# Kernel tuning notes

Hardware: AMD Instinct MI355X
Metric: run time of the kernel (lower is better)

Reference implementation:

```python
import jax, jax.numpy as jnp
import numpy as np

N_NODES = 100000


def _deg_isqrt(idx, n):
    # clamped-to-1 degree, then ^-0.5 (DGL GraphConv norm='both')
    deg = jax.ops.segment_sum(jnp.ones(idx.shape, jnp.float32), idx, num_segments=n)
    return jnp.power(jnp.maximum(deg, 1.0), -0.5)


def _graph_conv(feat, W, b, src, dst, out_isqrt, in_isqrt, n):
    # norm='both': scale by src out-degree^-1/2, mult-first (in>out), spmm, scale by dst in-degree^-1/2
    h = (feat * out_isqrt[:, None]) @ W                      # [N, out]
    h = jax.ops.segment_sum(h[src], dst, num_segments=n)     # gather/scatter over edges
    return h * in_isqrt[:, None] + b


def setup_inputs() -> dict:
    key = jax.random.key(0)
    ks = jax.random.split(key, 10)
    in_dim, h1, h2 = 512, 64, 32
    n, e = N_NODES, 800000
    features = jax.random.normal(ks[0], (n, in_dim), jnp.float32)
    src = jax.random.randint(ks[1], (e,), 0, n)
    dst = jax.random.randint(ks[2], (e,), 0, n)
    noise = jax.random.normal(ks[3], (n, h2), jnp.float32)
    s1 = 1.0 / np.sqrt(in_dim)
    s2 = 1.0 / np.sqrt(h1)
    W1 = jax.random.uniform(ks[4], (in_dim, h1), jnp.float32, -s1, s1)
    b1 = jnp.zeros((h1,), jnp.float32)
    W2 = jax.random.uniform(ks[5], (h1, h2), jnp.float32, -s2, s2)
    b2 = jnp.zeros((h2,), jnp.float32)
    W3 = jax.random.uniform(ks[6], (h1, h2), jnp.float32, -s2, s2)
    b3 = jnp.zeros((h2,), jnp.float32)
    return {"features": features, "src": src, "dst": dst, "noise": noise,
            "W1": W1, "b1": b1, "W2": W2, "b2": b2, "W3": W3, "b3": b3}


def reference(features, src, dst, noise, W1, b1, W2, b2, W3, b3):
    n = features.shape[0]
    out_isqrt = _deg_isqrt(src, n)
    in_isqrt = _deg_isqrt(dst, n)
    h = jax.nn.relu(_graph_conv(features, W1, b1, src, dst, out_isqrt, in_isqrt, n))
    mean = _graph_conv(h, W2, b2, src, dst, out_isqrt, in_isqrt, n)
    log_std = _graph_conv(h, W3, b3, src, dst, out_isqrt, in_isqrt, n)
    z = mean + noise * jnp.exp(log_std)
    return z, mean, log_std
```

## Files before the change

kernel.cpp:

```cpp
#include <hip/hip_runtime.h>
#include <hip/hip_bf16.h>


typedef __attribute__((ext_vector_type(8))) short short8;
typedef __attribute__((ext_vector_type(4))) float f32x4;
typedef unsigned short ushort_t;

static __device__ inline short f2bf(float f)
{
    union { __hip_bfloat16 h; short s; } u;
    u.h = __float2bfloat16(f);
    return u.s;
}

static __device__ inline float bf2f(ushort_t u)
{
    union { float f; unsigned v; } w;
    w.v = ((unsigned)u) << 16;
    return w.f;
}

static __device__ inline short8 cvt8(float4 lo, float4 hi)
{
    short8 r;
    r[0] = f2bf(lo.x); r[1] = f2bf(lo.y); r[2] = f2bf(lo.z); r[3] = f2bf(lo.w);
    r[4] = f2bf(hi.x); r[5] = f2bf(hi.y); r[6] = f2bf(hi.z); r[7] = f2bf(hi.w);
    return r;
}

__global__ __launch_bounds__(256) void k_setup(
    const float* __restrict__ W1, const float* __restrict__ W2,
    const float* __restrict__ W3, short* __restrict__ w1f,
    float* __restrict__ wc, int4* __restrict__ zp, int z4)
{
    int gid = blockIdx.x * 256 + threadIdx.x;
    if (gid < z4) zp[gid] = make_int4(0, 0, 0, 0);
    if (gid < 64 * 64) {
        int k = gid >> 6, c = gid & 63;
        wc[gid] = (c < 32) ? W2[k * 32 + c] : W3[k * 32 + (c - 32)];
    }
    if (gid < 512 * 64) {
        int k = gid >> 6, c = gid & 63;
        int kt = k >> 5, kk = k & 31, nt = c >> 4, lr = c & 15;
        int kg = kk >> 3, j = kk & 7;
        int l = kg * 16 + lr;
        w1f[(kt * 4 + nt) * 512 + l * 8 + j] = f2bf(W1[gid]);
    }
}

__global__ __launch_bounds__(256) void k_deg_int(
    const int* __restrict__ src, const int* __restrict__ dst,
    int* __restrict__ degS, int* __restrict__ degD, int e)
{
    int gid = blockIdx.x * 256 + threadIdx.x;
    if (gid >= e) return;
    atomicAdd(&degS[src[gid]], 1);
    atomicAdd(&degD[dst[gid]], 1);
}

__global__ __launch_bounds__(256) void k_scan_block_sums(
    const int* __restrict__ deg, int* __restrict__ partials, int n)
{
    __shared__ int red[256];
    int gid = blockIdx.x * 256 + threadIdx.x;
    red[threadIdx.x] = (gid < n) ? deg[gid] : 0;
    __syncthreads();
    for (int s = 128; s > 0; s >>= 1) {
        if (threadIdx.x < s) red[threadIdx.x] += red[threadIdx.x + s];
        __syncthreads();
    }
    if (threadIdx.x == 0) partials[blockIdx.x] = red[0];
}

__global__ __launch_bounds__(512) void k_scan_partials(
    int* __restrict__ partials, int nb)
{
    __shared__ int s[512];
    int t = threadIdx.x;
    s[t] = (t < nb) ? partials[t] : 0;
    __syncthreads();
    for (int d = 1; d < 512; d <<= 1) {
        int v = (t >= d) ? s[t - d] : 0;
        __syncthreads();
        s[t] += v;
        __syncthreads();
    }
    if (t < nb) partials[t] = (t == 0) ? 0 : s[t - 1];
}

__global__ __launch_bounds__(256) void k_scan_final(
    const int* __restrict__ degD, const int* __restrict__ degS,
    const int* __restrict__ partials,
    int* __restrict__ row_ptr, int* __restrict__ cursor,
    float* __restrict__ isq_out, float* __restrict__ isq_in, int n)
{
    __shared__ int s[256];
    int t = threadIdx.x;
    int gid = blockIdx.x * 256 + t;
    int v = (gid < n) ? degD[gid] : 0;
    s[t] = v;
    __syncthreads();
    for (int d = 1; d < 256; d <<= 1) {
        int u = (t >= d) ? s[t - d] : 0;
        __syncthreads();
        s[t] += u;
        __syncthreads();
    }
    int start = partials[blockIdx.x] + s[t] - v;
    if (gid < n) {
        row_ptr[gid] = start;
        cursor[gid]  = start;
        isq_in[gid]  = 1.0f / sqrtf((float)max(v, 1));
        isq_out[gid] = 1.0f / sqrtf((float)max(degS[gid], 1));
    }
    if (gid == n - 1) row_ptr[n] = start + v;
}

__global__ __launch_bounds__(256) void k_scatter(
    const int* __restrict__ src, const int* __restrict__ dst,
    int* __restrict__ cursor, int* __restrict__ edge_src, int e)
{
    int gid = blockIdx.x * 256 + threadIdx.x;
    if (gid >= e) return;
    int pos = atomicAdd(&cursor[dst[gid]], 1);
    edge_src[pos] = src[gid];
}

__global__ __launch_bounds__(256) void k_gemm1_mfma(
    const float* __restrict__ X, const short* __restrict__ w1f,
    const float* __restrict__ scale, ushort_t* __restrict__ Y, int n)
{
    const int tid  = threadIdx.x;
    const int l    = tid & 63;
    const int wv   = tid >> 6;
    const int row0 = blockIdx.x * 128 + wv * 32;
    const int lr   = l & 15;
    const int kg   = l >> 4;

    int ra0 = row0 + lr;       if (ra0 >= n) ra0 = n - 1;
    int ra1 = row0 + 16 + lr;  if (ra1 >= n) ra1 = n - 1;
    const float* pa0 = X + (size_t)ra0 * 512 + kg * 8;
    const float* pa1 = X + (size_t)ra1 * 512 + kg * 8;
    const short* pb  = w1f + l * 8;

    f32x4 acc[2][4];
#pragma unroll
    for (int i = 0; i < 2; ++i)
#pragma unroll
        for (int j = 0; j < 4; ++j) acc[i][j] = (f32x4){0.f, 0.f, 0.f, 0.f};

    float4 a0lo = *(const float4*)(pa0);
    float4 a0hi = *(const float4*)(pa0 + 4);
    float4 a1lo = *(const float4*)(pa1);
    float4 a1hi = *(const float4*)(pa1 + 4);
    short8 b0 = *(const short8*)(pb);
    short8 b1 = *(const short8*)(pb + 512);
    short8 b2 = *(const short8*)(pb + 1024);
    short8 b3 = *(const short8*)(pb + 1536);

    for (int kt = 0; kt < 16; ++kt) {
        short8 ca0 = cvt8(a0lo, a0hi);
        short8 ca1 = cvt8(a1lo, a1hi);
        short8 cb0 = b0, cb1 = b1, cb2 = b2, cb3 = b3;

        if (kt < 15) {
            const float* q0 = pa0 + (kt + 1) * 32;
            const float* q1 = pa1 + (kt + 1) * 32;
            a0lo = *(const float4*)(q0);
            a0hi = *(const float4*)(q0 + 4);
            a1lo = *(const float4*)(q1);
            a1hi = *(const float4*)(q1 + 4);
            const short* q = pb + (size_t)(kt + 1) * 2048;
            b0 = *(const short8*)(q);
            b1 = *(const short8*)(q + 512);
            b2 = *(const short8*)(q + 1024);
            b3 = *(const short8*)(q + 1536);
        }

        acc[0][0] = __builtin_amdgcn_mfma_f32_16x16x32_bf16(ca0, cb0, acc[0][0], 0, 0, 0);
        acc[0][1] = __builtin_amdgcn_mfma_f32_16x16x32_bf16(ca0, cb1, acc[0][1], 0, 0, 0);
        acc[0][2] = __builtin_amdgcn_mfma_f32_16x16x32_bf16(ca0, cb2, acc[0][2], 0, 0, 0);
        acc[0][3] = __builtin_amdgcn_mfma_f32_16x16x32_bf16(ca0, cb3, acc[0][3], 0, 0, 0);
        acc[1][0] = __builtin_amdgcn_mfma_f32_16x16x32_bf16(ca1, cb0, acc[1][0], 0, 0, 0);
        acc[1][1] = __builtin_amdgcn_mfma_f32_16x16x32_bf16(ca1, cb1, acc[1][1], 0, 0, 0);
        acc[1][2] = __builtin_amdgcn_mfma_f32_16x16x32_bf16(ca1, cb2, acc[1][2], 0, 0, 0);
        acc[1][3] = __builtin_amdgcn_mfma_f32_16x16x32_bf16(ca1, cb3, acc[1][3], 0, 0, 0);
    }

#pragma unroll
    for (int mr = 0; mr < 2; ++mr) {
#pragma unroll
        for (int m = 0; m < 4; ++m) {
            int row = row0 + mr * 16 + kg * 4 + m;
            if (row < n) {
                float s = scale[row];
#pragma unroll
                for (int nt = 0; nt < 4; ++nt)
                    Y[(size_t)row * 64 + nt * 16 + lr] =
                        (ushort_t)f2bf(acc[mr][nt][m] * s);
            }
        }
    }
}

__global__ __launch_bounds__(256) void k_gather_h(
    const int* __restrict__ row_ptr, const int* __restrict__ edge_src,
    const ushort_t* __restrict__ x, const float* __restrict__ isq_in,
    const float* __restrict__ isq_out, const float* __restrict__ b1,
    float* __restrict__ h, int n)
{
    int col  = threadIdx.x & 63;
    int node = __builtin_amdgcn_readfirstlane(blockIdx.x * 4 + (threadIdx.x >> 6));
    if (node >= n) return;
    int j = row_ptr[node], jend = row_ptr[node + 1];
    float a0 = 0.f, a1 = 0.f, a2 = 0.f, a3 = 0.f;
    float a4 = 0.f, a5 = 0.f, a6 = 0.f, a7 = 0.f;
    for (; j + 7 < jend; j += 8) {
        int e0 = edge_src[j],     e1 = edge_src[j + 1];
        int e2 = edge_src[j + 2], e3 = edge_src[j + 3];
        int e4 = edge_src[j + 4], e5 = edge_src[j + 5];
        int e6 = edge_src[j + 6], e7 = edge_src[j + 7];
        a0 += bf2f(x[(size_t)e0 * 64 + col]);
        a1 += bf2f(x[(size_t)e1 * 64 + col]);
        a2 += bf2f(x[(size_t)e2 * 64 + col]);
        a3 += bf2f(x[(size_t)e3 * 64 + col]);
        a4 += bf2f(x[(size_t)e4 * 64 + col]);
        a5 += bf2f(x[(size_t)e5 * 64 + col]);
        a6 += bf2f(x[(size_t)e6 * 64 + col]);
        a7 += bf2f(x[(size_t)e7 * 64 + col]);
    }
    for (; j + 1 < jend; j += 2) {
        int e0 = edge_src[j], e1 = edge_src[j + 1];
        a0 += bf2f(x[(size_t)e0 * 64 + col]);
        a1 += bf2f(x[(size_t)e1 * 64 + col]);
    }
    if (j < jend) a2 += bf2f(x[(size_t)edge_src[j] * 64 + col]);
    float acc = ((a0 + a1) + (a2 + a3)) + ((a4 + a5) + (a6 + a7));
    h[(size_t)node * 64 + col] =
        fmaxf(acc * isq_in[node] + b1[col], 0.f) * isq_out[node];
}

__global__ __launch_bounds__(256) void k_gemm2(
    const float* __restrict__ X, const float* __restrict__ W,
    ushort_t* __restrict__ Y, int n)
{
    __shared__ float sx[64][68];
    __shared__ float sw[64][64];
    const int tid  = threadIdx.x;
    const int colp = tid & 31;
    const int rg   = tid >> 5;
    const int row0 = blockIdx.x * 64;

    float2 acc[8];
#pragma unroll
    for (int i = 0; i < 8; ++i) acc[i] = make_float2(0.f, 0.f);

#pragma unroll
    for (int p = 0; p < 4; ++p) {
        int u = p * 256 + tid;
        int r = u >> 4, c4 = (u & 15) * 4;
        int row = row0 + r;
        float4 v = make_float4(0.f, 0.f, 0.f, 0.f);
        if (row < n) v = *(const float4*)&X[(size_t)row * 64 + c4];
        *(float4*)&sx[r][c4] = v;
        *(float4*)&sw[r][c4] = *(const float4*)&W[u * 4];
    }
    __syncthreads();

#pragma unroll 4
    for (int k4 = 0; k4 < 64; k4 += 4) {
        float2 w0 = *(const float2*)&sw[k4 + 0][colp * 2];
        float2 w1 = *(const float2*)&sw[k4 + 1][colp * 2];
        float2 w2 = *(const float2*)&sw[k4 + 2][colp * 2];
        float2 w3 = *(const float2*)&sw[k4 + 3][colp * 2];
#pragma unroll
        for (int i = 0; i < 8; ++i) {
            float4 f = *(const float4*)&sx[rg * 8 + i][k4];
            acc[i].x += f.x * w0.x + f.y * w1.x + f.z * w2.x + f.w * w3.x;
            acc[i].y += f.x * w0.y + f.y * w1.y + f.z * w2.y + f.w * w3.y;
        }
    }

#pragma unroll
    for (int i = 0; i < 8; ++i) {
        int row = row0 + rg * 8 + i;
        if (row < n) {
            unsigned lo = (unsigned)(unsigned short)f2bf(acc[i].x);
            unsigned hi = (unsigned)(unsigned short)f2bf(acc[i].y);
            ((unsigned*)Y)[(size_t)row * 32 + colp] = (hi << 16) | lo;
        }
    }
}

__global__ __launch_bounds__(256) void k_gather_final(
    const int* __restrict__ row_ptr, const int* __restrict__ edge_src,
    const ushort_t* __restrict__ t23, const float* __restrict__ isq_in,
    const float* __restrict__ b2, const float* __restrict__ b3,
    const float* __restrict__ noise, float* __restrict__ out, int n)
{
    int lane = threadIdx.x & 63;
    int node = __builtin_amdgcn_readfirstlane(blockIdx.x * 4 + (threadIdx.x >> 6));
    if (node >= n) return;
    int j = row_ptr[node], jend = row_ptr[node + 1];
    float a0 = 0.f, a1 = 0.f, a2 = 0.f, a3 = 0.f;
    float a4 = 0.f, a5 = 0.f, a6 = 0.f, a7 = 0.f;
    for (; j + 7 < jend; j += 8) {
        int e0 = edge_src[j],     e1 = edge_src[j + 1];
        int e2 = edge_src[j + 2], e3 = edge_src[j + 3];
        int e4 = edge_src[j + 4], e5 = edge_src[j + 5];
        int e6 = edge_src[j + 6], e7 = edge_src[j + 7];
        a0 += bf2f(t23[(size_t)e0 * 64 + lane]);
        a1 += bf2f(t23[(size_t)e1 * 64 + lane]);
        a2 += bf2f(t23[(size_t)e2 * 64 + lane]);
        a3 += bf2f(t23[(size_t)e3 * 64 + lane]);
        a4 += bf2f(t23[(size_t)e4 * 64 + lane]);
        a5 += bf2f(t23[(size_t)e5 * 64 + lane]);
        a6 += bf2f(t23[(size_t)e6 * 64 + lane]);
        a7 += bf2f(t23[(size_t)e7 * 64 + lane]);
    }
    for (; j + 1 < jend; j += 2) {
        int e0 = edge_src[j], e1 = edge_src[j + 1];
        a0 += bf2f(t23[(size_t)e0 * 64 + lane]);
        a1 += bf2f(t23[(size_t)e1 * 64 + lane]);
    }
    if (j < jend) a2 += bf2f(t23[(size_t)edge_src[j] * 64 + lane]);
    float acc = ((a0 + a1) + (a2 + a3)) + ((a4 + a5) + (a6 + a7));
    float si = isq_in[node];
    float v  = acc * si + (lane < 32 ? b2[lane] : b3[lane - 32]);
    float lv = __shfl(v, lane | 32, 64);
    int total = n * 32;
    int base  = node * 32 + (lane & 31);
    if (lane < 32) {
        float z = v + noise[base] * expf(lv);
        out[base]         = z;
        out[total + base] = v;
    } else {
        out[2 * total + base] = v;
    }
}

extern "C" void kernel_launch(void* const* d_in, const int* in_sizes, int n_in,
                              void* d_out, int out_size, void* d_ws, size_t ws_size,
                              hipStream_t stream)
{
    const float* feat  = (const float*)d_in[0];
    const int*   src   = (const int*)d_in[1];
    const int*   dst   = (const int*)d_in[2];
    const float* noise = (const float*)d_in[3];
    const float* W1    = (const float*)d_in[4];
    const float* b1    = (const float*)d_in[5];
    const float* W2    = (const float*)d_in[6];
    const float* b2    = (const float*)d_in[7];
    const float* W3    = (const float*)d_in[8];
    const float* b3    = (const float*)d_in[9];

    const int n = in_sizes[0] / 512;
    const int e = in_sizes[1];

    float* ws      = (float*)d_ws;
    float* isq_out = ws;
    float* isq_in  = ws + n;
    float* bufA    = ws + 2 * (size_t)n;
    float* bufB    = bufA + 64 * (size_t)n;
    float* wc      = bufB + 64 * (size_t)n;
    short* w1f     = (short*)(wc + 64 * 64);
    int*   ip      = (int*)(w1f + 512 * 64);
    int* row_ptr   = ip;
    int* cursor    = ip + (n + 1);
    int* partials  = cursor + n;
    int* edge_src  = partials + 512;
    int* degS = (int*)bufA;
    int* degD = degS + n;
    float* out = (float*)d_out;

    const int nb = (n + 255) / 256;
    const int z4 = (2 * n) / 4;

    k_setup<<<(z4 + 255) / 256, 256, 0, stream>>>(
        W1, W2, W3, w1f, wc, (int4*)degS, z4);

    k_deg_int<<<(e + 255) / 256, 256, 0, stream>>>(src, dst, degS, degD, e);

    k_scan_block_sums<<<nb, 256, 0, stream>>>(degD, partials, n);
    k_scan_partials<<<1, 512, 0, stream>>>(partials, nb);
    k_scan_final<<<nb, 256, 0, stream>>>(
        degD, degS, partials, row_ptr, cursor, isq_out, isq_in, n);
    k_scatter<<<(e + 255) / 256, 256, 0, stream>>>(src, dst, cursor, edge_src, e);

    k_gemm1_mfma<<<(n + 127) / 128, 256, 0, stream>>>(
        feat, w1f, isq_out, (ushort_t*)bufA, n);

    k_gather_h<<<(n + 3) / 4, 256, 0, stream>>>(
        row_ptr, edge_src, (const ushort_t*)bufA, isq_in, isq_out, b1, bufB, n);

    k_gemm2<<<(n + 63) / 64, 256, 0, stream>>>(bufB, wc, (ushort_t*)bufA, n);

    k_gather_final<<<(n + 3) / 4, 256, 0, stream>>>(
        row_ptr, edge_src, (const ushort_t*)bufA, isq_in, b2, b3, noise, out, n);
}
```

Baseline: 282.0 us.

## Halve rows per wave in gemm1, double-buffer A loads, hoist gather scalar loads

The first MFMA GEMM now gives each wave 16 rows instead of 32 and launches twice as many blocks. It also prefetches A two K-steps ahead using alternating register buffers and fully unrolls the K loop. The aim is more waves and deeper load pipelining for the bandwidth-bound 512-wide feature read. In the gather kernels, per-node scale, bias and noise loads move ahead of the edge loop so their latency overlaps the gathers. The trade-off is that each B-operand (W1) load is now reused over half as many rows, which raises weight traffic per output row.

```diff
diff --git a/kernel.cpp b/kernel.cpp
--- a/kernel.cpp
+++ b/kernel.cpp
@@ -133,72 +133,58 @@
     const int tid  = threadIdx.x;
     const int l    = tid & 63;
     const int wv   = tid >> 6;
-    const int row0 = blockIdx.x * 128 + wv * 32;
+    const int row0 = (blockIdx.x * 4 + wv) * 16;
     const int lr   = l & 15;
     const int kg   = l >> 4;
 
-    int ra0 = row0 + lr;       if (ra0 >= n) ra0 = n - 1;
-    int ra1 = row0 + 16 + lr;  if (ra1 >= n) ra1 = n - 1;
-    const float* pa0 = X + (size_t)ra0 * 512 + kg * 8;
-    const float* pa1 = X + (size_t)ra1 * 512 + kg * 8;
-    const short* pb  = w1f + l * 8;
-
-    f32x4 acc[2][4];
-#pragma unroll
-    for (int i = 0; i < 2; ++i)
-#pragma unroll
-        for (int j = 0; j < 4; ++j) acc[i][j] = (f32x4){0.f, 0.f, 0.f, 0.f};
-
-    float4 a0lo = *(const float4*)(pa0);
-    float4 a0hi = *(const float4*)(pa0 + 4);
-    float4 a1lo = *(const float4*)(pa1);
-    float4 a1hi = *(const float4*)(pa1 + 4);
+    int ra = row0 + lr;  if (ra >= n) ra = n - 1;
+    const float* pa = X + (size_t)ra * 512 + kg * 8;
+    const short* pb = w1f + l * 8;
+
+    f32x4 acc[4];
+#pragma unroll
+    for (int j = 0; j < 4; ++j) acc[j] = (f32x4){0.f, 0.f, 0.f, 0.f};
+
+    float4 alo0 = *(const float4*)(pa);
+    float4 ahi0 = *(const float4*)(pa + 4);
+    float4 alo1 = *(const float4*)(pa + 32);
+    float4 ahi1 = *(const float4*)(pa + 36);
     short8 b0 = *(const short8*)(pb);
     short8 b1 = *(const short8*)(pb + 512);
     short8 b2 = *(const short8*)(pb + 1024);
     short8 b3 = *(const short8*)(pb + 1536);
 
+#pragma unroll
     for (int kt = 0; kt < 16; ++kt) {
-        short8 ca0 = cvt8(a0lo, a0hi);
-        short8 ca1 = cvt8(a1lo, a1hi);
+        short8 ca = (kt & 1) ? cvt8(alo1, ahi1) : cvt8(alo0, ahi0);
+        if (kt + 2 < 16) {
+            const float* q = pa + (kt + 2) * 32;
+            if (kt & 1) { alo1 = *(const float4*)(q); ahi1 = *(const float4*)(q + 4); }
+            else        { alo0 = *(const float4*)(q); ahi0 = *(const float4*)(q + 4); }
+        }
         short8 cb0 = b0, cb1 = b1, cb2 = b2, cb3 = b3;
-
-        if (kt < 15) {
-            const float* q0 = pa0 + (kt + 1) * 32;
-            const float* q1 = pa1 + (kt + 1) * 32;
-            a0lo = *(const float4*)(q0);
-            a0hi = *(const float4*)(q0 + 4);
-            a1lo = *(const float4*)(q1);
-            a1hi = *(const float4*)(q1 + 4);
+        if (kt + 1 < 16) {
             const short* q = pb + (size_t)(kt + 1) * 2048;
             b0 = *(const short8*)(q);
             b1 = *(const short8*)(q + 512);
             b2 = *(const short8*)(q + 1024);
             b3 = *(const short8*)(q + 1536);
         }
-
-        acc[0][0] = __builtin_amdgcn_mfma_f32_16x16x32_bf16(ca0, cb0, acc[0][0], 0, 0, 0);
-        acc[0][1] = __builtin_amdgcn_mfma_f32_16x16x32_bf16(ca0, cb1, acc[0][1], 0, 0, 0);
-        acc[0][2] = __builtin_amdgcn_mfma_f32_16x16x32_bf16(ca0, cb2, acc[0][2], 0, 0, 0);
-        acc[0][3] = __builtin_amdgcn_mfma_f32_16x16x32_bf16(ca0, cb3, acc[0][3], 0, 0, 0);
-        acc[1][0] = __builtin_amdgcn_mfma_f32_16x16x32_bf16(ca1, cb0, acc[1][0], 0, 0, 0);
-        acc[1][1] = __builtin_amdgcn_mfma_f32_16x16x32_bf16(ca1, cb1, acc[1][1], 0, 0, 0);
-        acc[1][2] = __builtin_amdgcn_mfma_f32_16x16x32_bf16(ca1, cb2, acc[1][2], 0, 0, 0);
-        acc[1][3] = __builtin_amdgcn_mfma_f32_16x16x32_bf16(ca1, cb3, acc[1][3], 0, 0, 0);
-    }
-
-#pragma unroll
-    for (int mr = 0; mr < 2; ++mr) {
-#pragma unroll
-        for (int m = 0; m < 4; ++m) {
-            int row = row0 + mr * 16 + kg * 4 + m;
-            if (row < n) {
-                float s = scale[row];
-#pragma unroll
-                for (int nt = 0; nt < 4; ++nt)
-                    Y[(size_t)row * 64 + nt * 16 + lr] =
-                        (ushort_t)f2bf(acc[mr][nt][m] * s);
-            }
+        acc[0] = __builtin_amdgcn_mfma_f32_16x16x32_bf16(ca, cb0, acc[0], 0, 0, 0);
+        acc[1] = __builtin_amdgcn_mfma_f32_16x16x32_bf16(ca, cb1, acc[1], 0, 0, 0);
+        acc[2] = __builtin_amdgcn_mfma_f32_16x16x32_bf16(ca, cb2, acc[2], 0, 0, 0);
+        acc[3] = __builtin_amdgcn_mfma_f32_16x16x32_bf16(ca, cb3, acc[3], 0, 0, 0);
+    }
+
+#pragma unroll
+    for (int m = 0; m < 4; ++m) {
+        int row = row0 + kg * 4 + m;
+        if (row < n) {
+            float s = scale[row];
+#pragma unroll
+            for (int nt = 0; nt < 4; ++nt)
+                Y[(size_t)row * 64 + nt * 16 + lr] =
+                    (ushort_t)f2bf(acc[nt][m] * s);
         }
     }
 }
@@ -212,6 +198,9 @@
     int col  = threadIdx.x & 63;
     int node = __builtin_amdgcn_readfirstlane(blockIdx.x * 4 + (threadIdx.x >> 6));
     if (node >= n) return;
+    float si = isq_in[node];
+    float so = isq_out[node];
+    float bb = b1[col];
     int j = row_ptr[node], jend = row_ptr[node + 1];
     float a0 = 0.f, a1 = 0.f, a2 = 0.f, a3 = 0.f;
     float a4 = 0.f, a5 = 0.f, a6 = 0.f, a7 = 0.f;
@@ -236,8 +225,7 @@
     }
     if (j < jend) a2 += bf2f(x[(size_t)edge_src[j] * 64 + col]);
     float acc = ((a0 + a1) + (a2 + a3)) + ((a4 + a5) + (a6 + a7));
-    h[(size_t)node * 64 + col] =
-        fmaxf(acc * isq_in[node] + b1[col], 0.f) * isq_out[node];
+    h[(size_t)node * 64 + col] = fmaxf(acc * si + bb, 0.f) * so;
 }
 
 __global__ __launch_bounds__(256) void k_gemm2(
@@ -301,6 +289,11 @@
     int lane = threadIdx.x & 63;
     int node = __builtin_amdgcn_readfirstlane(blockIdx.x * 4 + (threadIdx.x >> 6));
     if (node >= n) return;
+    float si   = isq_in[node];
+    float bias = (lane < 32) ? b2[lane] : b3[lane - 32];
+    int total  = n * 32;
+    int base   = node * 32 + (lane & 31);
+    float nz   = (lane < 32) ? noise[base] : 0.f;
     int j = row_ptr[node], jend = row_ptr[node + 1];
     float a0 = 0.f, a1 = 0.f, a2 = 0.f, a3 = 0.f;
     float a4 = 0.f, a5 = 0.f, a6 = 0.f, a7 = 0.f;
@@ -325,13 +318,10 @@
     }
     if (j < jend) a2 += bf2f(t23[(size_t)edge_src[j] * 64 + lane]);
     float acc = ((a0 + a1) + (a2 + a3)) + ((a4 + a5) + (a6 + a7));
-    float si = isq_in[node];
-    float v  = acc * si + (lane < 32 ? b2[lane] : b3[lane - 32]);
+    float v  = acc * si + bias;
     float lv = __shfl(v, lane | 32, 64);
-    int total = n * 32;
-    int base  = node * 32 + (lane & 31);
     if (lane < 32) {
-        float z = v + noise[base] * expf(lv);
+        float z = v + nz * expf(lv);
         out[base]         = z;
         out[total + base] = v;
     } else {
@@ -387,7 +377,7 @@
         degD, degS, partials, row_ptr, cursor, isq_out, isq_in, n);
     k_scatter<<<(e + 255) / 256, 256, 0, stream>>>(src, dst, cursor, edge_src, e);
 
-    k_gemm1_mfma<<<(n + 127) / 128, 256, 0, stream>>>(
+    k_gemm1_mfma<<<(n + 63) / 64, 256, 0, stream>>>(
         feat, w1f, isq_out, (ushort_t*)bufA, n);
 
     k_gather_h<<<(n + 3) / 4, 256, 0, stream>>>(
```

Result: faster. 266.4 us (-5.5%).
